# Kernel tuning notes

Measured on AMD Instinct MI355X. Metric: run time of the kernel, lower is better.

The kernel has to match this reference:

```python
import jax, jax.numpy as jnp
import numpy as np

S = 2048      # seq_len
E = 1024      # embedding_size
H = 16        # attn_head
D = E // H    # per-head dim = 64
EPS = 1e-5


def _layernorm(x, g, b):
    mu = jnp.mean(x, axis=-1, keepdims=True)
    var = jnp.var(x, axis=-1, keepdims=True)
    return (x - mu) * jax.lax.rsqrt(var + EPS) * g + b


def setup_inputs() -> dict:
    key = jax.random.key(0)
    ks = jax.random.split(key, 16)
    s = 1.0 / np.sqrt(E)
    inp = {
        "x_word_emb": jax.random.normal(ks[0], (S, E), jnp.float32),
        "x_pos_emb": jax.random.normal(ks[1], (S, E), jnp.float32),
        # stacked per-head projections: weight [H, E, D], bias [H, D]
        "Wq": jax.random.uniform(ks[2], (H, E, D), jnp.float32, -s, s),
        "bq": jax.random.uniform(ks[3], (H, D), jnp.float32, -s, s),
        "Wk": jax.random.uniform(ks[4], (H, E, D), jnp.float32, -s, s),
        "bk": jax.random.uniform(ks[5], (H, D), jnp.float32, -s, s),
        "Wv": jax.random.uniform(ks[6], (H, E, D), jnp.float32, -s, s),
        "bv": jax.random.uniform(ks[7], (H, D), jnp.float32, -s, s),
        "W0": jax.random.uniform(ks[8], (E, E), jnp.float32, -s, s),
        "b0": jax.random.uniform(ks[9], (E,), jnp.float32, -s, s),
        "g1": jnp.ones((E,), jnp.float32),
        "be1": jnp.zeros((E,), jnp.float32),
        "W1": jax.random.uniform(ks[10], (4 * E, E), jnp.float32, -s, s),
        "b1": jax.random.uniform(ks[11], (4 * E,), jnp.float32, -s, s),
        "W2": jax.random.uniform(ks[12], (E, 4 * E), jnp.float32, -1.0 / np.sqrt(4 * E), 1.0 / np.sqrt(4 * E)),
        "b2": jax.random.uniform(ks[13], (E,), jnp.float32, -1.0 / np.sqrt(4 * E), 1.0 / np.sqrt(4 * E)),
        "g2": jnp.ones((E,), jnp.float32),
        "be2": jnp.zeros((E,), jnp.float32),
    }
    return inp


def reference(x_word_emb, x_pos_emb, Wq, bq, Wk, bk, Wv, bv,
              W0, b0, g1, be1, W1, b1, W2, b2, g2, be2):
    emb = x_word_emb + x_pos_emb                            # [S, E]
    # batched per-head projections (equivalent to the per-head Linear loop)
    q = jnp.einsum('se,hed->hsd', emb, Wq) + bq[:, None, :]  # [H, S, D]
    k = jnp.einsum('se,hed->hsd', emb, Wk) + bk[:, None, :]
    v = jnp.einsum('se,hed->hsd', emb, Wv) + bv[:, None, :]
    scores = jnp.einsum('hsd,htd->hst', q, k)               # [H, S, S]
    # original: F.softmax(z).data -> weights detached (no grad through q/k)
    w = jax.lax.stop_gradient(jax.nn.softmax(scores, axis=-1))
    # NOTE: original scales AFTER softmax@V, not on the logits
    z = jnp.einsum('hst,htd->hsd', w, v) / np.sqrt(D)       # [H, S, D]
    # concat heads along feature dim in head order
    z = jnp.transpose(z, (1, 0, 2)).reshape(S, E)           # [S, E]
    z = z @ W0.T + b0
    out1 = _layernorm(z + emb, g1, be1)
    out2 = jax.nn.relu(out1 @ W1.T + b1)                    # [S, 4E]
    out2 = out2 @ W2.T + b2
    return _layernorm(out1 + out2, g2, be2)
```

## Files before the change

kernel.cpp:

```cpp
#include <hip/hip_runtime.h>

#define SLEN 2048
#define EDIM 1024
#define HNUM 16
#define DDIM 64

typedef unsigned short u16;
typedef unsigned int u32;
typedef __attribute__((ext_vector_type(8))) __bf16 bf16x8;
typedef __attribute__((ext_vector_type(2))) __bf16 bf16x2;
typedef __attribute__((ext_vector_type(4))) float f32x4;

__device__ __forceinline__ u16 f2bf(float f) {
  u32 u = __builtin_bit_cast(u32, f);
  u = (u + 0x7fffu + ((u >> 16) & 1u)) >> 16;
  return (u16)u;
}

__device__ __forceinline__ u32 packbf(float a, float b) {
  bf16x2 t; t[0] = (__bf16)a; t[1] = (__bf16)b;
  return __builtin_bit_cast(u32, t);
}

__device__ __forceinline__ void gload_lds16(const void* g, void* l) {
  __builtin_amdgcn_global_load_lds(
      (const __attribute__((address_space(1))) void*)g,
      (__attribute__((address_space(3))) void*)l, 16, 0, 0);
}

__device__ __forceinline__ u32 swz(u32 b) { return b ^ (((b >> 7) & 7u) << 4); }

template<int MODE>
__global__ __launch_bounds__(256, 2) void gemm_bt(
    const u16* __restrict__ A, const u16* __restrict__ Bt,
    const float* __restrict__ bias, const float* __restrict__ add,
    void* __restrict__ outp, int M, int N, int K)
{
  __shared__ __align__(16) u16 As[128 * 64];
  __shared__ __align__(16) u16 Bs[128 * 64];
  const int t = threadIdx.x;
  const int lane = t & 63, wv = t >> 6;
  const int bm = blockIdx.y * 128, bn = blockIdx.x * 128;
  const int wm = (wv >> 1) * 64, wn = (wv & 1) * 64;
  f32x4 acc[4][4] = {};

  const char* Ab = (const char*)A;
  const char* Bb = (const char*)Bt;

  for (int k0 = 0; k0 < K; k0 += 64) {
    __syncthreads();
#pragma unroll
    for (int j = 0; j < 4; ++j) {
      u32 bp = (u32)t * 16u + (u32)j * 4096u;
      u32 L = swz(bp);
      u32 row = L >> 7, colb = L & 127u;
      gload_lds16(Ab + ((size_t)(bm + row) * K + k0) * 2 + colb, (char*)As + bp);
      gload_lds16(Bb + ((size_t)(bn + row) * K + k0) * 2 + colb, (char*)Bs + bp);
    }
    __syncthreads();
#pragma unroll
    for (int ks = 0; ks < 2; ++ks) {
      bf16x8 af[4], bfr[4];
#pragma unroll
      for (int i = 0; i < 4; ++i) {
        u32 ra = (u32)(wm + i * 16 + (lane & 15));
        u32 La = (ra << 7) + (u32)ks * 64u + (u32)(lane >> 4) * 16u;
        af[i] = *(const bf16x8*)((const char*)As + (La ^ ((ra & 7u) << 4)));
        u32 rb = (u32)(wn + i * 16 + (lane & 15));
        u32 Lb = (rb << 7) + (u32)ks * 64u + (u32)(lane >> 4) * 16u;
        bfr[i] = *(const bf16x8*)((const char*)Bs + (Lb ^ ((rb & 7u) << 4)));
      }
#pragma unroll
      for (int mi = 0; mi < 4; ++mi)
#pragma unroll
        for (int ni = 0; ni < 4; ++ni)
          acc[mi][ni] = __builtin_amdgcn_mfma_f32_16x16x32_bf16(af[mi], bfr[ni], acc[mi][ni], 0, 0, 0);
    }
  }

  const int cr = (lane >> 4) * 4, cc = lane & 15;
#pragma unroll
  for (int ni = 0; ni < 4; ++ni) {
    const int col = bn + wn + ni * 16 + cc;
    const float bvv = bias[col];
#pragma unroll
    for (int mi = 0; mi < 4; ++mi) {
#pragma unroll
      for (int r = 0; r < 4; ++r) {
        const int row = bm + wm + mi * 16 + cr + r;
        float v = acc[mi][ni][r] + bvv;
        const size_t idx = (size_t)row * N + col;
        if constexpr (MODE == 0) ((u16*)outp)[idx] = f2bf(v);
        else if constexpr (MODE == 1) ((u16*)outp)[idx] = f2bf(v > 0.f ? v : 0.f);
        else ((float*)outp)[idx] = v + add[idx];
      }
    }
  }
}

template<int MODE>
__global__ __launch_bounds__(256, 4) void gemm_bt64(
    const u16* __restrict__ A, const u16* __restrict__ Bt,
    const float* __restrict__ bias, float* __restrict__ part1,
    void* __restrict__ outp, int M, int N, int lda, int KS)
{
  __shared__ __align__(16) u16 As[64 * 64];
  __shared__ __align__(16) u16 Bs[128 * 64];
  const int t = threadIdx.x;
  const int lane = t & 63, wv = t >> 6;
  const int bm = blockIdx.y * 64, bn = blockIdx.x * 128;
  const int wm = (wv >> 1) * 32, wn = (wv & 1) * 64;
  const int koff = blockIdx.z * KS;
  f32x4 acc[2][4] = {};

  const char* Ab = (const char*)A;
  const char* Bb = (const char*)Bt;

  for (int k0 = koff; k0 < koff + KS; k0 += 64) {
    __syncthreads();
    {
      u32 bp = (u32)t * 16u;
      u32 L = swz(bp);
      u32 row = L >> 7, colb = L & 127u;
      gload_lds16(Ab + ((size_t)(bm + row) * lda + k0) * 2 + colb, (char*)As + bp);
      u32 bp2 = bp + 4096u;
      u32 L2 = swz(bp2);
      u32 row2 = L2 >> 7, colb2 = L2 & 127u;
      gload_lds16(Ab + ((size_t)(bm + row2) * lda + k0) * 2 + colb2, (char*)As + bp2);
    }
#pragma unroll
    for (int j = 0; j < 4; ++j) {
      u32 bp = (u32)t * 16u + (u32)j * 4096u;
      u32 L = swz(bp);
      u32 row = L >> 7, colb = L & 127u;
      gload_lds16(Bb + ((size_t)(bn + row) * lda + k0) * 2 + colb, (char*)Bs + bp);
    }
    __syncthreads();
#pragma unroll
    for (int ks = 0; ks < 2; ++ks) {
      bf16x8 af[2], bfr[4];
#pragma unroll
      for (int i = 0; i < 2; ++i) {
        u32 ra = (u32)(wm + i * 16 + (lane & 15));
        u32 La = (ra << 7) + (u32)ks * 64u + (u32)(lane >> 4) * 16u;
        af[i] = *(const bf16x8*)((const char*)As + (La ^ ((ra & 7u) << 4)));
      }
#pragma unroll
      for (int i = 0; i < 4; ++i) {
        u32 rb = (u32)(wn + i * 16 + (lane & 15));
        u32 Lb = (rb << 7) + (u32)ks * 64u + (u32)(lane >> 4) * 16u;
        bfr[i] = *(const bf16x8*)((const char*)Bs + (Lb ^ ((rb & 7u) << 4)));
      }
#pragma unroll
      for (int mi = 0; mi < 2; ++mi)
#pragma unroll
        for (int ni = 0; ni < 4; ++ni)
          acc[mi][ni] = __builtin_amdgcn_mfma_f32_16x16x32_bf16(af[mi], bfr[ni], acc[mi][ni], 0, 0, 0);
    }
  }

  float* po = (MODE == 3 && blockIdx.z) ? part1 : (float*)outp;
  const int cr = (lane >> 4) * 4, cc = lane & 15;
#pragma unroll
  for (int ni = 0; ni < 4; ++ni) {
    const int col = bn + wn + ni * 16 + cc;
    const float bvv = (MODE == 3) ? 0.f : bias[col];
#pragma unroll
    for (int mi = 0; mi < 2; ++mi) {
#pragma unroll
      for (int r = 0; r < 4; ++r) {
        const int row = bm + wm + mi * 16 + cr + r;
        float v = acc[mi][ni][r] + bvv;
        const size_t idx = (size_t)row * N + col;
        if constexpr (MODE == 0) ((u16*)outp)[idx] = f2bf(v);
        else if constexpr (MODE == 1) ((u16*)outp)[idx] = f2bf(v > 0.f ? v : 0.f);
        else po[idx] = v;
      }
    }
  }
}

__global__ __launch_bounds__(256) void red2_kernel(
    const float4* __restrict__ pA, const float4* __restrict__ pB,
    const float* __restrict__ bias, const float4* __restrict__ add,
    float4* __restrict__ out)
{
  const int i = blockIdx.x * 256 + threadIdx.x;
  float4 a = pA[i], b = pB[i], c = add[i];
  float4 g = ((const float4*)bias)[i & 255];
  float4 o;
  o.x = a.x + b.x + c.x + g.x;
  o.y = a.y + b.y + c.y + g.y;
  o.z = a.z + b.z + c.z + g.z;
  o.w = a.w + b.w + c.w + g.w;
  out[i] = o;
}

__global__ __launch_bounds__(256, 2) void attn_kernel(
    const u16* __restrict__ qkv, const u16* __restrict__ vt, u16* __restrict__ zcat)
{
  __shared__ __align__(16) char lds[32768];
  const int t = threadIdx.x, lane = t & 63;
  const int g = lane >> 4, qi = lane & 15;
  const int wv = t >> 6;
  const int h = blockIdx.y;
  const int q0 = blockIdx.x * 64 + wv * 16;

  bf16x8 qf[2];
#pragma unroll
  for (int ds = 0; ds < 2; ++ds)
    qf[ds] = *(const bf16x8*)(qkv + (size_t)(q0 + qi) * 3072 + h * 64 + ds * 32 + g * 8);

  const char* kgp[2];
  const char* vgp[2];
  u32 ldo[2];
#pragma unroll
  for (int j = 0; j < 2; ++j) {
    u32 bp = (u32)t * 16u + (u32)j * 4096u;
    u32 L = swz(bp);
    u32 row = L >> 7, colb = L & 127u;
    kgp[j] = (const char*)qkv + ((size_t)row * 3072 + 1024 + h * 64) * 2 + colb;
    vgp[j] = (const char*)vt + ((size_t)(h * 64 + row)) * (SLEN * 2) + colb;
    ldo[j] = bp;
  }

  f32x4 zacc[4] = {};
  float m = -1e30f, l = 0.f;

  const int NT = SLEN / 64;
  {
    char* base = lds;
#pragma unroll
    for (int j = 0; j < 2; ++j) {
      gload_lds16(kgp[j], base + ldo[j]);
      gload_lds16(vgp[j] + 0, base + 8192 + ldo[j]);
    }
  }
  __syncthreads();

  int cur = 0;
  for (int kt = 0; kt < NT; ++kt) {
    if (kt + 1 < NT) {
      char* base = lds + (cur ^ 1) * 16384;
      size_t ko = (size_t)(kt + 1) * (64 * 3072 * 2);
      int vo = (kt + 1) * 128;
#pragma unroll
      for (int j = 0; j < 2; ++j) {
        gload_lds16(kgp[j] + ko, base + ldo[j]);
        gload_lds16(vgp[j] + vo, base + 8192 + ldo[j]);
      }
    }

    const char* Kl = lds + cur * 16384;
    const char* Vl = Kl + 8192;

    float p[4][4];
#pragma unroll
    for (int kcg = 0; kcg < 4; ++kcg) {
      f32x4 s = {};
#pragma unroll
      for (int ds = 0; ds < 2; ++ds) {
        u32 rk = (u32)(kcg * 16 + qi);
        u32 L = (rk << 7) + (u32)ds * 64u + (u32)g * 16u;
        bf16x8 kf = *(const bf16x8*)(Kl + (L ^ ((rk & 7u) << 4)));
        s = __builtin_amdgcn_mfma_f32_16x16x32_bf16(kf, qf[ds], s, 0, 0, 0);
      }
#pragma unroll
      for (int r = 0; r < 4; ++r) p[kcg][r] = s[r];
    }

    float tmax = p[0][0];
#pragma unroll
    for (int kcg = 0; kcg < 4; ++kcg)
#pragma unroll
      for (int r = 0; r < 4; ++r) tmax = fmaxf(tmax, p[kcg][r]);
    tmax = fmaxf(tmax, __shfl_xor(tmax, 16));
    tmax = fmaxf(tmax, __shfl_xor(tmax, 32));

    float newm = fmaxf(m, tmax);
    float scl = __expf(m - newm);
    float psum = 0.f;
    u32 pk[4][2];
#pragma unroll
    for (int kcg = 0; kcg < 4; ++kcg) {
#pragma unroll
      for (int r = 0; r < 4; ++r) {
        float e = __expf(p[kcg][r] - newm);
        p[kcg][r] = e;
        psum += e;
      }
      pk[kcg][0] = packbf(p[kcg][0], p[kcg][1]);
      pk[kcg][1] = packbf(p[kcg][2], p[kcg][3]);
    }
    psum += __shfl_xor(psum, 16);
    psum += __shfl_xor(psum, 32);
    l = l * scl + psum;
    m = newm;
#pragma unroll
    for (int ni = 0; ni < 4; ++ni)
#pragma unroll
      for (int r = 0; r < 4; ++r) zacc[ni][r] *= scl;

#pragma unroll
    for (int ks = 0; ks < 2; ++ks) {
      u32 w[4];
#pragma unroll
      for (int wi = 0; wi < 4; ++wi) {
        const int src = qi + 16 * (2 * (g & 1) + (wi >> 1));
        u32 wa = (u32)__shfl((int)pk[2 * ks][wi & 1], src);
        u32 wb = (u32)__shfl((int)pk[2 * ks + 1][wi & 1], src);
        w[wi] = (g & 2) ? wb : wa;
      }
      uint4 wp = {w[0], w[1], w[2], w[3]};
      bf16x8 pb = __builtin_bit_cast(bf16x8, wp);
#pragma unroll
      for (int ni = 0; ni < 4; ++ni) {
        u32 rv = (u32)(ni * 16 + qi);
        u32 L = (rv << 7) + (u32)ks * 64u + (u32)g * 16u;
        bf16x8 vf = *(const bf16x8*)(Vl + (L ^ ((rv & 7u) << 4)));
        zacc[ni] = __builtin_amdgcn_mfma_f32_16x16x32_bf16(vf, pb, zacc[ni], 0, 0, 0);
      }
    }

    __syncthreads();
    cur ^= 1;
  }

  const float inv = 0.125f / l;
#pragma unroll
  for (int ni = 0; ni < 4; ++ni) {
    u32 a = packbf(zacc[ni][0] * inv, zacc[ni][1] * inv);
    u32 b = packbf(zacc[ni][2] * inv, zacc[ni][3] * inv);
    uint2 st = {a, b};
    *(uint2*)(zcat + (size_t)(q0 + qi) * EDIM + h * 64 + ni * 16 + g * 4) = st;
  }
}

__global__ __launch_bounds__(256) void ln_kernel(
    const float* __restrict__ in, const float* __restrict__ g, const float* __restrict__ b,
    float* __restrict__ outf, u16* __restrict__ outb)
{
  const int row = blockIdx.x, t = threadIdx.x;
  const float4* rp = (const float4*)(in + (size_t)row * EDIM);
  float4 x = rp[t];
  float s = x.x + x.y + x.z + x.w;
  float sq = x.x * x.x + x.y * x.y + x.z * x.z + x.w * x.w;
#pragma unroll
  for (int m = 1; m < 64; m <<= 1) { s += __shfl_xor(s, m); sq += __shfl_xor(sq, m); }
  __shared__ float red[8];
  const int wv = t >> 6, lane = t & 63;
  if (lane == 0) { red[wv] = s; red[4 + wv] = sq; }
  __syncthreads();
  s = red[0] + red[1] + red[2] + red[3];
  sq = red[4] + red[5] + red[6] + red[7];
  const float mu = s * (1.f / EDIM);
  const float rs = rsqrtf(sq * (1.f / EDIM) - mu * mu + 1e-5f);
  float4 gg = ((const float4*)g)[t];
  float4 bb = ((const float4*)b)[t];
  float4 y;
  y.x = (x.x - mu) * rs * gg.x + bb.x;
  y.y = (x.y - mu) * rs * gg.y + bb.y;
  y.z = (x.z - mu) * rs * gg.z + bb.z;
  y.w = (x.w - mu) * rs * gg.w + bb.w;
  if (outf) ((float4*)(outf + (size_t)row * EDIM))[t] = y;
  if (outb) {
    uint2 pkv;
    pkv.x = (u32)f2bf(y.x) | ((u32)f2bf(y.y) << 16);
    pkv.y = (u32)f2bf(y.z) | ((u32)f2bf(y.w) << 16);
    ((uint2*)(outb + (size_t)row * EDIM))[t] = pkv;
  }
}

__global__ void emb_kernel(const float4* __restrict__ a, const float4* __restrict__ b,
                           float4* __restrict__ ef, uint2* __restrict__ eb)
{
  const int i = blockIdx.x * 256 + threadIdx.x;
  float4 x = a[i], y = b[i];
  float4 e; e.x = x.x + y.x; e.y = x.y + y.y; e.z = x.z + y.z; e.w = x.w + y.w;
  ef[i] = e;
  uint2 pk;
  pk.x = (u32)f2bf(e.x) | ((u32)f2bf(e.y) << 16);
  pk.y = (u32)f2bf(e.z) | ((u32)f2bf(e.w) << 16);
  eb[i] = pk;
}

__global__ void cvt_kernel(const float4* __restrict__ in, uint2* __restrict__ out, int n4)
{
  const int i = blockIdx.x * 256 + threadIdx.x;
  if (i >= n4) return;
  float4 x = in[i];
  uint2 pk;
  pk.x = (u32)f2bf(x.x) | ((u32)f2bf(x.y) << 16);
  pk.y = (u32)f2bf(x.z) | ((u32)f2bf(x.w) << 16);
  out[i] = pk;
}

__global__ void bias3_kernel(const float* __restrict__ bq, const float* __restrict__ bk,
                             const float* __restrict__ bv, float* __restrict__ o)
{
  const int i = blockIdx.x * 256 + threadIdx.x;
  if (i >= 3072) return;
  o[i] = i < 1024 ? bq[i] : (i < 2048 ? bk[i - 1024] : bv[i - 2048]);
}

__global__ __launch_bounds__(256) void wqkv_kernel(
    const float* __restrict__ Wq, const float* __restrict__ Wk, const float* __restrict__ Wv,
    u16* __restrict__ outw)
{
  __shared__ float tile[64][65];
  const int et = blockIdx.x, h = blockIdx.y, wsel = blockIdx.z;
  const float* W = wsel == 0 ? Wq : (wsel == 1 ? Wk : Wv);
  const float* src = W + ((size_t)h * EDIM + et * 64) * DDIM;
  const int t = threadIdx.x;
#pragma unroll
  for (int it = 0; it < 4; ++it) {
    int fi = (t + it * 256) * 4;
    float4 v = *(const float4*)(src + fi);
    int e = fi >> 6, d = fi & 63;
    tile[e][d] = v.x; tile[e][d + 1] = v.y; tile[e][d + 2] = v.z; tile[e][d + 3] = v.w;
  }
  __syncthreads();
  const int d = t >> 2, ec = (t & 3) * 16;
  u16* dst = outw + ((size_t)(wsel * HNUM + h) * 64 + d) * EDIM + et * 64 + ec;
#pragma unroll
  for (int i = 0; i < 16; i += 2) {
    u32 p = (u32)f2bf(tile[ec + i][d]) | ((u32)f2bf(tile[ec + i + 1][d]) << 16);
    *(u32*)(dst + i) = p;
  }
}

__global__ __launch_bounds__(256) void vt_kernel(const u16* __restrict__ qkv, u16* __restrict__ vt)
{
  __shared__ __align__(16) u16 tile[64][80];
  const int st = blockIdx.x, h = blockIdx.y, t = threadIdx.x;
  const int sr = t >> 2, dc = (t & 3) * 16;
  const u16* src = qkv + (size_t)(st * 64 + sr) * 3072 + 2048 + h * 64 + dc;
  *(uint4*)&tile[sr][dc] = *(const uint4*)src;
  *(uint4*)&tile[sr][dc + 8] = *(const uint4*)(src + 8);
  __syncthreads();
  const int d = t >> 2, sc = (t & 3) * 16;
  u16* dst = vt + ((size_t)h * 64 + d) * SLEN + st * 64 + sc;
#pragma unroll
  for (int i = 0; i < 16; i += 2) {
    u32 p = (u32)tile[sc + i][d] | ((u32)tile[sc + i + 1][d] << 16);
    *(u32*)(dst + i) = p;
  }
}

extern "C" void kernel_launch(void* const* d_in, const int* in_sizes, int n_in,
                              void* d_out, int out_size, void* d_ws, size_t ws_size,
                              hipStream_t stream) {
  const float* xw  = (const float*)d_in[0];
  const float* xp  = (const float*)d_in[1];
  const float* Wq  = (const float*)d_in[2];
  const float* bq  = (const float*)d_in[3];
  const float* Wk  = (const float*)d_in[4];
  const float* bk  = (const float*)d_in[5];
  const float* Wv  = (const float*)d_in[6];
  const float* bv  = (const float*)d_in[7];
  const float* W0  = (const float*)d_in[8];
  const float* b0  = (const float*)d_in[9];
  const float* g1  = (const float*)d_in[10];
  const float* be1 = (const float*)d_in[11];
  const float* W1  = (const float*)d_in[12];
  const float* b1  = (const float*)d_in[13];
  const float* W2  = (const float*)d_in[14];
  const float* b2  = (const float*)d_in[15];
  const float* g2  = (const float*)d_in[16];
  const float* be2 = (const float*)d_in[17];
  float* out = (float*)d_out;
  char* ws = (char*)d_ws;

  const size_t MB = 1ull << 20;
  float* embf32 = (float*)(ws + 0);
  u16*   embf16 = (u16*)(ws + 8 * MB);
  u16*   zcat   = (u16*)(ws + 8 * MB);
  float* res2   = (float*)(ws + 8 * MB);
  u16*   Wqkvt  = (u16*)(ws + 12 * MB);
  u16*   h1     = (u16*)(ws + 12 * MB);
  u16*   QKV    = (u16*)(ws + 18 * MB);
  float* w0pA   = (float*)(ws + 18 * MB);
  float* w0pB   = (float*)(ws + 26 * MB);
  u16*   Vt     = (u16*)(ws + 30 * MB);
  float* res1   = (float*)(ws + 34 * MB);
  float* out1f  = (float*)(ws + 34 * MB);
  u16*   out1b  = (u16*)(ws + 42 * MB);
  float* w2pB   = (float*)(ws + 42 * MB);
  u16*   W0b    = (u16*)(ws + 46 * MB);
  u16*   W1b    = (u16*)(ws + 48 * MB);
  u16*   W2b    = (u16*)(ws + 56 * MB);
  float* w2pA   = (float*)(ws + 0);
  float* bias3  = (float*)(ws + 64 * MB);

  emb_kernel<<<2048, 256, 0, stream>>>((const float4*)xw, (const float4*)xp,
                                       (float4*)embf32, (uint2*)embf16);
  cvt_kernel<<<1024, 256, 0, stream>>>((const float4*)W0, (uint2*)W0b, 1024 * 1024 / 4);
  cvt_kernel<<<4096, 256, 0, stream>>>((const float4*)W1, (uint2*)W1b, 4096 * 1024 / 4);
  cvt_kernel<<<4096, 256, 0, stream>>>((const float4*)W2, (uint2*)W2b, 1024 * 4096 / 4);
  bias3_kernel<<<12, 256, 0, stream>>>(bq, bk, bv, bias3);
  wqkv_kernel<<<dim3(16, 16, 3), 256, 0, stream>>>(Wq, Wk, Wv, Wqkvt);

  gemm_bt64<0><<<dim3(3072 / 128, 2048 / 64, 1), 256, 0, stream>>>(
      embf16, Wqkvt, bias3, nullptr, QKV, SLEN, 3072, 1024, 1024);

  vt_kernel<<<dim3(32, 16), 256, 0, stream>>>(QKV, Vt);

  attn_kernel<<<dim3(SLEN / 64, HNUM), 256, 0, stream>>>(QKV, Vt, zcat);

  gemm_bt64<3><<<dim3(1024 / 128, 2048 / 64, 2), 256, 0, stream>>>(
      zcat, W0b, nullptr, w0pB, w0pA, SLEN, 1024, 1024, 512);
  red2_kernel<<<2048, 256, 0, stream>>>((const float4*)w0pA, (const float4*)w0pB,
                                        b0, (const float4*)embf32, (float4*)res1);

  ln_kernel<<<SLEN, 256, 0, stream>>>(res1, g1, be1, out1f, out1b);

  gemm_bt<1><<<dim3(4096 / 128, 2048 / 128), 256, 0, stream>>>(
      out1b, W1b, b1, nullptr, h1, SLEN, 4096, 1024);

  gemm_bt64<3><<<dim3(1024 / 128, 2048 / 64, 2), 256, 0, stream>>>(
      h1, W2b, nullptr, w2pB, w2pA, SLEN, 1024, 4096, 2048);
  red2_kernel<<<2048, 256, 0, stream>>>((const float4*)w2pA, (const float4*)w2pB,
                                        b2, (const float4*)out1f, (float4*)res2);

  ln_kernel<<<SLEN, 256, 0, stream>>>(res2, g2, be2, out, nullptr);
}
```

Before: 190.6 us.

## Split attention over key range with flash-decoding style combine kernel

```diff
diff --git a/kernel.cpp b/kernel.cpp
--- a/kernel.cpp
+++ b/kernel.cpp
@@ -15,6 +15,11 @@
   u32 u = __builtin_bit_cast(u32, f);
   u = (u + 0x7fffu + ((u >> 16) & 1u)) >> 16;
   return (u16)u;
+}
+
+__device__ __forceinline__ float bf2f(u16 v) {
+  u32 u = ((u32)v) << 16;
+  return __builtin_bit_cast(float, u);
 }
 
 __device__ __forceinline__ u32 packbf(float a, float b) {
@@ -196,8 +201,9 @@
   out[i] = o;
 }
 
-__global__ __launch_bounds__(256, 2) void attn_kernel(
-    const u16* __restrict__ qkv, const u16* __restrict__ vt, u16* __restrict__ zcat)
+__global__ __launch_bounds__(256, 4) void attn_kernel(
+    const u16* __restrict__ qkv, const u16* __restrict__ vt,
+    u16* __restrict__ zp, float2* __restrict__ mlb)
 {
   __shared__ __align__(16) char lds[32768];
   const int t = threadIdx.x, lane = t & 63;
@@ -205,6 +211,8 @@
   const int wv = t >> 6;
   const int h = blockIdx.y;
   const int q0 = blockIdx.x * 64 + wv * 16;
+  const int kt0 = blockIdx.z * (SLEN / 128);
+  const int ktE = kt0 + SLEN / 128;
 
   bf16x8 qf[2];
 #pragma unroll
@@ -227,20 +235,21 @@
   f32x4 zacc[4] = {};
   float m = -1e30f, l = 0.f;
 
-  const int NT = SLEN / 64;
   {
     char* base = lds;
+    size_t ko = (size_t)kt0 * (64 * 3072 * 2);
+    int vo = kt0 * 128;
 #pragma unroll
     for (int j = 0; j < 2; ++j) {
-      gload_lds16(kgp[j], base + ldo[j]);
-      gload_lds16(vgp[j] + 0, base + 8192 + ldo[j]);
+      gload_lds16(kgp[j] + ko, base + ldo[j]);
+      gload_lds16(vgp[j] + vo, base + 8192 + ldo[j]);
     }
   }
   __syncthreads();
 
   int cur = 0;
-  for (int kt = 0; kt < NT; ++kt) {
-    if (kt + 1 < NT) {
+  for (int kt = kt0; kt < ktE; ++kt) {
+    if (kt + 1 < ktE) {
       char* base = lds + (cur ^ 1) * 16384;
       size_t ko = (size_t)(kt + 1) * (64 * 3072 * 2);
       int vo = (kt + 1) * 128;
@@ -326,14 +335,43 @@
     cur ^= 1;
   }
 
-  const float inv = 0.125f / l;
+  const int bid = (h * 32 + blockIdx.x) * 2 + blockIdx.z;
+  u16* zb = zp + (size_t)bid * 4096;
 #pragma unroll
   for (int ni = 0; ni < 4; ++ni) {
-    u32 a = packbf(zacc[ni][0] * inv, zacc[ni][1] * inv);
-    u32 b = packbf(zacc[ni][2] * inv, zacc[ni][3] * inv);
+    u32 a = packbf(zacc[ni][0], zacc[ni][1]);
+    u32 b = packbf(zacc[ni][2], zacc[ni][3]);
     uint2 st = {a, b};
-    *(uint2*)(zcat + (size_t)(q0 + qi) * EDIM + h * 64 + ni * 16 + g * 4) = st;
-  }
+    *(uint2*)(zb + (size_t)(wv * 16 + qi) * 64 + ni * 16 + g * 4) = st;
+  }
+  if (g == 0) mlb[(size_t)bid * 64 + wv * 16 + qi] = make_float2(m, l);
+}
+
+__global__ __launch_bounds__(256) void comb_kernel(
+    const u16* __restrict__ zp, const float2* __restrict__ mlb, u16* __restrict__ zcat)
+{
+  const int flat = blockIdx.x * 256 + threadIdx.x;
+  const int d4 = flat & 15;
+  const int q = (flat >> 4) & 2047;
+  const int h = flat >> 15;
+  const int qt = q >> 6, qr = q & 63;
+  const size_t pb = (size_t)(h * 32 + qt) * 2;
+  const size_t base = pb * 4096 + (size_t)qr * 64 + d4 * 4;
+  uint2 a = *(const uint2*)(zp + base);
+  uint2 b = *(const uint2*)(zp + base + 4096);
+  float2 ml0 = mlb[pb * 64 + qr];
+  float2 ml1 = mlb[(pb + 1) * 64 + qr];
+  const float M = fmaxf(ml0.x, ml1.x);
+  const float e0 = __expf(ml0.x - M), e1 = __expf(ml1.x - M);
+  const float s = 0.125f / (e0 * ml0.y + e1 * ml1.y);
+  float o0 = (e0 * bf2f((u16)(a.x & 0xffff)) + e1 * bf2f((u16)(b.x & 0xffff))) * s;
+  float o1 = (e0 * bf2f((u16)(a.x >> 16))   + e1 * bf2f((u16)(b.x >> 16))) * s;
+  float o2 = (e0 * bf2f((u16)(a.y & 0xffff)) + e1 * bf2f((u16)(b.y & 0xffff))) * s;
+  float o3 = (e0 * bf2f((u16)(a.y >> 16))   + e1 * bf2f((u16)(b.y >> 16))) * s;
+  uint2 st;
+  st.x = (u32)f2bf(o0) | ((u32)f2bf(o1) << 16);
+  st.y = (u32)f2bf(o2) | ((u32)f2bf(o3) << 16);
+  *(uint2*)(zcat + (size_t)q * EDIM + h * 64 + d4 * 4) = st;
 }
 
 __global__ __launch_bounds__(256) void ln_kernel(
@@ -482,14 +520,16 @@
   float* w0pA   = (float*)(ws + 18 * MB);
   float* w0pB   = (float*)(ws + 26 * MB);
   u16*   Vt     = (u16*)(ws + 30 * MB);
+  u16*   zp     = (u16*)(ws + 34 * MB);
+  float2* mlb   = (float2*)(ws + 42 * MB);
   float* res1   = (float*)(ws + 34 * MB);
   float* out1f  = (float*)(ws + 34 * MB);
-  u16*   out1b  = (u16*)(ws + 42 * MB);
-  float* w2pB   = (float*)(ws + 42 * MB);
+  u16*   out1b  = (u16*)(ws + 28 * MB);
   u16*   W0b    = (u16*)(ws + 46 * MB);
   u16*   W1b    = (u16*)(ws + 48 * MB);
   u16*   W2b    = (u16*)(ws + 56 * MB);
   float* w2pA   = (float*)(ws + 0);
+  float* w2pB   = (float*)(ws + 48 * MB);
   float* bias3  = (float*)(ws + 64 * MB);
 
   emb_kernel<<<2048, 256, 0, stream>>>((const float4*)xw, (const float4*)xp,
@@ -505,7 +545,8 @@
 
   vt_kernel<<<dim3(32, 16), 256, 0, stream>>>(QKV, Vt);
 
-  attn_kernel<<<dim3(SLEN / 64, HNUM), 256, 0, stream>>>(QKV, Vt, zcat);
+  attn_kernel<<<dim3(SLEN / 64, HNUM, 2), 256, 0, stream>>>(QKV, Vt, zp, mlb);
+  comb_kernel<<<2048, 256, 0, stream>>>(zp, mlb, zcat);
 
   gemm_bt64<3><<<dim3(1024 / 128, 2048 / 64, 2), 256, 0, stream>>>(
       zcat, W0b, nullptr, w0pB, w0pA, SLEN, 1024, 1024, 512);
```

New measurement: 187.2 us. About the same (-1.8%).
